# Kernel tuning notes

Measured on AMD Instinct MI355X. Metric: run time of the kernel, lower is better.

The kernel has to match this reference:

```python
import jax, jax.numpy as jnp
import numpy as np

N = 50000
E = 800000
IN = 128
HEADS = 4
C = 32  # out_features per head
HC = HEADS * C


def setup_inputs() -> dict:
    key = jax.random.key(0)
    ks = jax.random.split(key, 10)
    s_in = 1.0 / np.sqrt(IN)
    x = jax.random.normal(ks[0], (N, IN), dtype=jnp.float32)
    edge_index = jax.random.randint(ks[1], (2, E), 0, N, dtype=jnp.int64)
    Wq = jax.random.normal(ks[2], (IN, HC), dtype=jnp.float32) * s_in
    bq = jnp.zeros((HC,), dtype=jnp.float32)
    Wk = jax.random.normal(ks[3], (IN, HC), dtype=jnp.float32) * s_in
    bk = jnp.zeros((HC,), dtype=jnp.float32)
    Wv = jax.random.normal(ks[4], (IN, HC), dtype=jnp.float32) * s_in
    bv = jnp.zeros((HC,), dtype=jnp.float32)
    Wskip = jax.random.normal(ks[5], (IN, HC), dtype=jnp.float32) * s_in
    bskip = jnp.zeros((HC,), dtype=jnp.float32)
    return {"x": x, "edge_index": edge_index, "Wq": Wq, "bq": bq,
            "Wk": Wk, "bk": bk, "Wv": Wv, "bv": bv,
            "Wskip": Wskip, "bskip": bskip}


def reference(x, edge_index, Wq, bq, Wk, bk, Wv, bv, Wskip, bskip):
    src = edge_index[0]  # message source j
    dst = edge_index[1]  # message target i

    q = (x @ Wq + bq).reshape(N, HEADS, C)
    k = (x @ Wk + bk).reshape(N, HEADS, C)
    v = (x @ Wv + bv).reshape(N, HEADS, C)

    # per-edge attention logits: [E, H]
    logits = jnp.einsum('ehc,ehc->eh', q[dst], k[src]) / jnp.sqrt(
        jnp.asarray(C, dtype=x.dtype))

    # segment softmax over incoming edges of each target node
    seg_max = jax.ops.segment_max(logits, dst, num_segments=N)
    seg_max = jnp.where(jnp.isfinite(seg_max), seg_max, 0.0)
    expd = jnp.exp(logits - seg_max[dst])
    seg_sum = jax.ops.segment_sum(expd, dst, num_segments=N)
    alpha = expd / (seg_sum[dst] + 1e-16)  # [E, H]

    # scatter-add weighted values: [N, H, C]
    msgs = alpha[:, :, None] * v[src]
    out = jax.ops.segment_sum(msgs, dst, num_segments=N)
    out = out.reshape(N, HC) + (x @ Wskip + bskip)  # root/skip connection

    # LeakyReLU(negative_slope=0.2)
    return jnp.where(out >= 0, out, 0.2 * out)
```

## Files before the change

### kernel.cpp

```cpp
#include <hip/hip_runtime.h>

#define N_NODES 50000
#define E_EDGES 800000
#define IN_F 128
#define HC 128
#define NCOLS 512
#define ROWTILES 3125
#define SCAN_BLOCKS 196
#define PACK_BLOCKS 32
#define HIST_BLOCKS ((E_EDGES + 255) / 256)

typedef __attribute__((ext_vector_type(8))) short short8;
typedef __attribute__((ext_vector_type(4))) float floatx4;

__device__ __forceinline__ unsigned short f2bf(float f) {
    union { float f; unsigned u; } x; x.f = f;
    unsigned r = x.u + 0x7FFF + ((x.u >> 16) & 1);
    return (unsigned short)(r >> 16);
}
__device__ __forceinline__ float bflo(unsigned u) {
    union { unsigned u; float f; } c; c.u = u << 16; return c.f;
}
__device__ __forceinline__ float bfhi(unsigned u) {
    union { unsigned u; float f; } c; c.u = u & 0xFFFF0000u; return c.f;
}

__global__ __launch_bounds__(256) void pack_w(
    const float* __restrict__ Wq, const float* __restrict__ Wk,
    const float* __restrict__ Wv, const float* __restrict__ Ws,
    const float* __restrict__ bq, const float* __restrict__ bk,
    const float* __restrict__ bv, const float* __restrict__ bs,
    short* __restrict__ bpack, float* __restrict__ bcat,
    int* __restrict__ cnt)
{
    int t = blockIdx.x * 256 + threadIdx.x;
    int lane = t & 63, ks = (t >> 6) & 3, nt = t >> 8;
    int col = nt * 16 + (lane & 15);
    int sec = col >> 7, c = col & 127;
    const float* W = sec == 0 ? Wq : sec == 1 ? Wk : sec == 2 ? Wv : Ws;
    int kbase = ks * 32 + (lane >> 4) * 8;
    short8 b;
#pragma unroll
    for (int j = 0; j < 8; j++) b[j] = (short)f2bf(W[(size_t)(kbase + j) * HC + c]);
    *(short8*)(bpack + (size_t)t * 8) = b;
    if (t < NCOLS) {
        int s2 = t >> 7, c2 = t & 127;
        bcat[t] = (s2 == 0 ? bq : s2 == 1 ? bk : s2 == 2 ? bv : bs)[c2];
    }
    for (int i = t; i < N_NODES; i += PACK_BLOCKS * 256) cnt[i] = 0;
}

__global__ __launch_bounds__(256) void gemm_hist(
    const float* __restrict__ x, const short* __restrict__ bpack,
    const float* __restrict__ bcat,
    unsigned short* __restrict__ q, unsigned short* __restrict__ k,
    unsigned short* __restrict__ v, float* __restrict__ out,
    const int* __restrict__ dst, int* __restrict__ cnt, int* __restrict__ rank)
{
    if (blockIdx.x >= ROWTILES) {
        int e = (blockIdx.x - ROWTILES) * 256 + threadIdx.x;
        if (e < E_EDGES) rank[e] = atomicAdd(&cnt[dst[e]], 1);
        return;
    }
    __shared__ __align__(16) unsigned char lds_raw[3 * 4096 + 8192];

    const int rt = blockIdx.x;
    const int cg = threadIdx.x >> 6;
    const int lane = threadIdx.x & 63;
    const int l16 = lane & 15;
    const int m0 = rt * 16 + l16;
    const int koff = (lane >> 4) * 8;

    short8 a0[4];
#pragma unroll
    for (int ks = 0; ks < 4; ks++) {
        const float* p0 = x + (size_t)m0 * IN_F + ks * 32 + koff;
        float4 lo = *(const float4*)p0;
        float4 hi = *(const float4*)(p0 + 4);
        short8 a;
        a[0] = (short)f2bf(lo.x); a[1] = (short)f2bf(lo.y);
        a[2] = (short)f2bf(lo.z); a[3] = (short)f2bf(lo.w);
        a[4] = (short)f2bf(hi.x); a[5] = (short)f2bf(hi.y);
        a[6] = (short)f2bf(hi.z); a[7] = (short)f2bf(hi.w);
        a0[ks] = a;
    }

    unsigned short* Lb = (unsigned short*)(lds_raw + cg * 4096);
    float*          Lf = (float*)(lds_raw + 12288);
    const int rrb = (lane >> 4) * 4;

#pragma unroll
    for (int nt8 = 0; nt8 < 8; nt8++) {
        const int nt = cg * 8 + nt8;
        floatx4 acc = {0.f, 0.f, 0.f, 0.f};
#pragma unroll
        for (int ks = 0; ks < 4; ks++) {
            short8 b = *(const short8*)(bpack + ((size_t)(nt * 4 + ks) * 64 + lane) * 8);
            acc = __builtin_amdgcn_mfma_f32_16x16x32_bf16(a0[ks], b, acc, 0, 0, 0);
        }
        const int c = nt8 * 16 + l16;
        const float bias = bcat[cg * 128 + c];
        if (cg < 3) {
#pragma unroll
            for (int r = 0; r < 4; r++)
                Lb[(rrb + r) * 128 + c] = f2bf(acc[r] + bias);
        } else {
#pragma unroll
            for (int r = 0; r < 4; r++)
                Lf[(rrb + r) * 128 + c] = acc[r] + bias;
        }
    }
    __syncthreads();

    if (cg < 3) {
        unsigned short* dstb = (cg == 0) ? q : (cg == 1) ? k : v;
        unsigned short* gout = dstb + (size_t)rt * 16 * HC;
#pragma unroll
        for (int rep = 0; rep < 4; rep++) {
            int idx = rep * 64 + lane;
            *(uint4*)(gout + idx * 8) = *(const uint4*)(Lb + idx * 8);
        }
    } else {
        float* gout = out + (size_t)rt * 16 * HC;
#pragma unroll
        for (int rep = 0; rep < 8; rep++) {
            int idx = rep * 64 + lane;
            *(float4*)(gout + idx * 4) = *(const float4*)(Lf + idx * 4);
        }
    }
}

__global__ __launch_bounds__(256) void scan_apply(const int* __restrict__ cnt,
                                                  int* __restrict__ rowptr)
{
    __shared__ int wsum[4];
    const int t = threadIdx.x;
    const int lane = t & 63, w = t >> 6;
    const int limit = blockIdx.x * 256;

    int s = 0;
    for (int i = t; i < limit; i += 256) s += cnt[i];
#pragma unroll
    for (int off = 32; off >= 1; off >>= 1) s += __shfl_xor(s, off);
    if (lane == 0) wsum[w] = s;
    __syncthreads();
    const int prefix = wsum[0] + wsum[1] + wsum[2] + wsum[3];
    __syncthreads();

    int idx = limit + t;
    int val = (idx < N_NODES) ? cnt[idx] : 0;
    int incl = val;
#pragma unroll
    for (int off = 1; off < 64; off <<= 1) {
        int u = __shfl_up(incl, off);
        if (lane >= off) incl += u;
    }
    if (lane == 63) wsum[w] = incl;
    __syncthreads();
    int pre = 0;
#pragma unroll
    for (int i = 0; i < 4; i++) if (i < w) pre += wsum[i];
    int excl = prefix + pre + incl - val;
    if (idx < N_NODES) rowptr[idx] = excl;
    if (idx == N_NODES - 1) rowptr[N_NODES] = E_EDGES;
}

__global__ __launch_bounds__(256) void scatter_k(const int* __restrict__ src,
                                                 const int* __restrict__ dst,
                                                 const int* __restrict__ rowptr,
                                                 const int* __restrict__ rank,
                                                 int* __restrict__ ssrc)
{
    int e = blockIdx.x * 256 + threadIdx.x;
    if (e < E_EDGES) ssrc[rowptr[dst[e]] + rank[e]] = src[e];
}

__global__ __launch_bounds__(256) void node_attn(
    const unsigned short* __restrict__ q, const unsigned short* __restrict__ k,
    const unsigned short* __restrict__ v, const int* __restrict__ rowptr,
    const int* __restrict__ ssrc, float* __restrict__ out)
{
    const int wave = (blockIdx.x * 256 + threadIdx.x) >> 6;
    if (wave >= N_NODES) return;
    const int lane = threadIdx.x & 63;
    const int node = wave;
    const int g = lane >> 3;
    const int l8 = lane & 7;
    const int c0 = l8 * 16;

    const uint4 uq0 = *(const uint4*)(q + (size_t)node * HC + c0);
    const uint4 uq1 = *(const uint4*)(q + (size_t)node * HC + c0 + 8);

    float acc[16];
#pragma unroll
    for (int i = 0; i < 16; i++) acc[i] = 0.f;
    float ssum = 0.f;

    const int beg = __builtin_amdgcn_readfirstlane(rowptr[node]);
    const int end = __builtin_amdgcn_readfirstlane(rowptr[node + 1]);
    const float scale = 0.17677669529663687f;

    for (int e = beg; e < end; e += 8) {
        const int ee = e + g;
        const int jj = ssrc[ee < end ? ee : beg];
        const unsigned short* kp = k + (size_t)jj * HC + c0;
        const unsigned short* vp = v + (size_t)jj * HC + c0;
        const uint4 uk0 = *(const uint4*)kp;
        const uint4 uk1 = *(const uint4*)(kp + 8);
        const uint4 uv0 = *(const uint4*)vp;
        const uint4 uv1 = *(const uint4*)(vp + 8);

        float p = bflo(uq0.x) * bflo(uk0.x) + bfhi(uq0.x) * bfhi(uk0.x)
                + bflo(uq0.y) * bflo(uk0.y) + bfhi(uq0.y) * bfhi(uk0.y)
                + bflo(uq0.z) * bflo(uk0.z) + bfhi(uq0.z) * bfhi(uk0.z)
                + bflo(uq0.w) * bflo(uk0.w) + bfhi(uq0.w) * bfhi(uk0.w)
                + bflo(uq1.x) * bflo(uk1.x) + bfhi(uq1.x) * bfhi(uk1.x)
                + bflo(uq1.y) * bflo(uk1.y) + bfhi(uq1.y) * bfhi(uk1.y)
                + bflo(uq1.z) * bflo(uk1.z) + bfhi(uq1.z) * bfhi(uk1.z)
                + bflo(uq1.w) * bflo(uk1.w) + bfhi(uq1.w) * bfhi(uk1.w);
        p += __shfl_xor(p, 1);
        float wgt = __expf(p * scale);
        wgt = (ee < end) ? wgt : 0.f;
        ssum += wgt;

        acc[0]  += wgt * bflo(uv0.x); acc[1]  += wgt * bfhi(uv0.x);
        acc[2]  += wgt * bflo(uv0.y); acc[3]  += wgt * bfhi(uv0.y);
        acc[4]  += wgt * bflo(uv0.z); acc[5]  += wgt * bfhi(uv0.z);
        acc[6]  += wgt * bflo(uv0.w); acc[7]  += wgt * bfhi(uv0.w);
        acc[8]  += wgt * bflo(uv1.x); acc[9]  += wgt * bfhi(uv1.x);
        acc[10] += wgt * bflo(uv1.y); acc[11] += wgt * bfhi(uv1.y);
        acc[12] += wgt * bflo(uv1.z); acc[13] += wgt * bfhi(uv1.z);
        acc[14] += wgt * bflo(uv1.w); acc[15] += wgt * bfhi(uv1.w);
    }

    ssum += __shfl_xor(ssum, 8);
    ssum += __shfl_xor(ssum, 16);
    ssum += __shfl_xor(ssum, 32);
#pragma unroll
    for (int i = 0; i < 16; i++) {
        acc[i] += __shfl_xor(acc[i], 8);
        acc[i] += __shfl_xor(acc[i], 16);
        acc[i] += __shfl_xor(acc[i], 32);
    }

    if (g == 0) {
        const float inv = 1.0f / (ssum + 1e-16f);
        float* op = out + (size_t)node * HC + c0;
        float o[16];
#pragma unroll
        for (int i = 0; i < 16; i += 4) {
            float4 s = *(const float4*)(op + i);
            o[i]     = acc[i]     * inv + s.x;
            o[i + 1] = acc[i + 1] * inv + s.y;
            o[i + 2] = acc[i + 2] * inv + s.z;
            o[i + 3] = acc[i + 3] * inv + s.w;
        }
#pragma unroll
        for (int i = 0; i < 16; i++) o[i] = o[i] >= 0.f ? o[i] : 0.2f * o[i];
#pragma unroll
        for (int i = 0; i < 16; i += 4)
            *(float4*)(op + i) = make_float4(o[i], o[i + 1], o[i + 2], o[i + 3]);
    }
}

extern "C" void kernel_launch(void* const* d_in, const int* in_sizes, int n_in,
                              void* d_out, int out_size, void* d_ws, size_t ws_size,
                              hipStream_t stream)
{
    const float* x    = (const float*)d_in[0];
    const int*   ei   = (const int*)d_in[1];
    const float* Wq   = (const float*)d_in[2];
    const float* bq   = (const float*)d_in[3];
    const float* Wk   = (const float*)d_in[4];
    const float* bk   = (const float*)d_in[5];
    const float* Wv   = (const float*)d_in[6];
    const float* bv   = (const float*)d_in[7];
    const float* Wsk  = (const float*)d_in[8];
    const float* bsk  = (const float*)d_in[9];
    float* out = (float*)d_out;

    char* w = (char*)d_ws;
    const size_t NFB = (size_t)N_NODES * HC * sizeof(unsigned short);
    unsigned short* q = (unsigned short*)w;            w += NFB;
    unsigned short* k = (unsigned short*)w;            w += NFB;
    unsigned short* v = (unsigned short*)w;            w += NFB;
    short* bpack = (short*)w;                          w += 8192 * 8 * sizeof(short);
    float* bcat  = (float*)w;                          w += NCOLS * sizeof(float);
    int* cnt    = (int*)w;                             w += N_NODES * sizeof(int);
    int* rowptr = (int*)w;                             w += (N_NODES + 1) * sizeof(int);
    int* rank   = (int*)w;                             w += (size_t)E_EDGES * sizeof(int);
    int* ssrc   = (int*)w;

    const int* srcIdx = ei;
    const int* dstIdx = ei + E_EDGES;

    pack_w<<<PACK_BLOCKS, 256, 0, stream>>>(Wq, Wk, Wv, Wsk, bq, bk, bv, bsk,
                                            bpack, bcat, cnt);
    gemm_hist<<<ROWTILES + HIST_BLOCKS, 256, 0, stream>>>(
        x, bpack, bcat, q, k, v, out, dstIdx, cnt, rank);
    scan_apply<<<SCAN_BLOCKS, 256, 0, stream>>>(cnt, rowptr);
    scatter_k<<<(E_EDGES + 255) / 256, 256, 0, stream>>>(srcIdx, dstIdx, rowptr, rank, ssrc);
    node_attn<<<(N_NODES * 64) / 256, 256, 0, stream>>>(q, k, v, rowptr, ssrc, out);
}
```

Before: 173.8 us.

## Process four row tiles per GEMM block and move histogram into pack kernel

The projection GEMM now handles four 16-row tiles per block, loading each packed weight fragment once and reusing it across four MFMA accumulators. The skip output is written straight from registers to global memory instead of staging through LDS. The edge histogram moves into the weight-pack kernel, and the count array is cleared with a memset instead. This reduces repeated weight loads and the number of blocks, but raises register pressure and makes the fp32 output stores uncoalesced.

Result: slower. 187.4 us (+7.8%).

```diff
diff --git a/kernel.cpp b/kernel.cpp
--- a/kernel.cpp
+++ b/kernel.cpp
@@ -6,6 +6,8 @@
 #define HC 128
 #define NCOLS 512
 #define ROWTILES 3125
+#define RT_PER_BLK 4
+#define GEMM_BLOCKS 782
 #define SCAN_BLOCKS 196
 #define PACK_BLOCKS 32
 #define HIST_BLOCKS ((E_EDGES + 255) / 256)
@@ -25,107 +27,119 @@
     union { unsigned u; float f; } c; c.u = u & 0xFFFF0000u; return c.f;
 }
 
-__global__ __launch_bounds__(256) void pack_w(
+__global__ __launch_bounds__(256) void pack_hist_k(
     const float* __restrict__ Wq, const float* __restrict__ Wk,
     const float* __restrict__ Wv, const float* __restrict__ Ws,
     const float* __restrict__ bq, const float* __restrict__ bk,
     const float* __restrict__ bv, const float* __restrict__ bs,
     short* __restrict__ bpack, float* __restrict__ bcat,
-    int* __restrict__ cnt)
-{
-    int t = blockIdx.x * 256 + threadIdx.x;
-    int lane = t & 63, ks = (t >> 6) & 3, nt = t >> 8;
-    int col = nt * 16 + (lane & 15);
-    int sec = col >> 7, c = col & 127;
-    const float* W = sec == 0 ? Wq : sec == 1 ? Wk : sec == 2 ? Wv : Ws;
-    int kbase = ks * 32 + (lane >> 4) * 8;
-    short8 b;
-#pragma unroll
-    for (int j = 0; j < 8; j++) b[j] = (short)f2bf(W[(size_t)(kbase + j) * HC + c]);
-    *(short8*)(bpack + (size_t)t * 8) = b;
-    if (t < NCOLS) {
-        int s2 = t >> 7, c2 = t & 127;
-        bcat[t] = (s2 == 0 ? bq : s2 == 1 ? bk : s2 == 2 ? bv : bs)[c2];
-    }
-    for (int i = t; i < N_NODES; i += PACK_BLOCKS * 256) cnt[i] = 0;
-}
-
-__global__ __launch_bounds__(256) void gemm_hist(
+    const int* __restrict__ dst, int* __restrict__ cnt, int* __restrict__ rank)
+{
+    if (blockIdx.x < PACK_BLOCKS) {
+        int t = blockIdx.x * 256 + threadIdx.x;
+        int lane = t & 63, ks = (t >> 6) & 3, nt = t >> 8;
+        int col = nt * 16 + (lane & 15);
+        int sec = col >> 7, c = col & 127;
+        const float* W = sec == 0 ? Wq : sec == 1 ? Wk : sec == 2 ? Wv : Ws;
+        int kbase = ks * 32 + (lane >> 4) * 8;
+        short8 b;
+#pragma unroll
+        for (int j = 0; j < 8; j++) b[j] = (short)f2bf(W[(size_t)(kbase + j) * HC + c]);
+        *(short8*)(bpack + (size_t)t * 8) = b;
+        if (t < NCOLS) {
+            int s2 = t >> 7, c2 = t & 127;
+            bcat[t] = (s2 == 0 ? bq : s2 == 1 ? bk : s2 == 2 ? bv : bs)[c2];
+        }
+    } else {
+        int e = (blockIdx.x - PACK_BLOCKS) * 256 + threadIdx.x;
+        if (e < E_EDGES) rank[e] = atomicAdd(&cnt[dst[e]], 1);
+    }
+}
+
+__global__ __launch_bounds__(256, 3) void gemm_mfma(
     const float* __restrict__ x, const short* __restrict__ bpack,
     const float* __restrict__ bcat,
     unsigned short* __restrict__ q, unsigned short* __restrict__ k,
-    unsigned short* __restrict__ v, float* __restrict__ out,
-    const int* __restrict__ dst, int* __restrict__ cnt, int* __restrict__ rank)
-{
-    if (blockIdx.x >= ROWTILES) {
-        int e = (blockIdx.x - ROWTILES) * 256 + threadIdx.x;
-        if (e < E_EDGES) rank[e] = atomicAdd(&cnt[dst[e]], 1);
-        return;
-    }
-    __shared__ __align__(16) unsigned char lds_raw[3 * 4096 + 8192];
-
-    const int rt = blockIdx.x;
+    unsigned short* __restrict__ v, float* __restrict__ out)
+{
+    __shared__ unsigned short Lb[3][RT_PER_BLK][16 * 128];
+
     const int cg = threadIdx.x >> 6;
     const int lane = threadIdx.x & 63;
     const int l16 = lane & 15;
-    const int m0 = rt * 16 + l16;
     const int koff = (lane >> 4) * 8;
-
-    short8 a0[4];
-#pragma unroll
-    for (int ks = 0; ks < 4; ks++) {
-        const float* p0 = x + (size_t)m0 * IN_F + ks * 32 + koff;
-        float4 lo = *(const float4*)p0;
-        float4 hi = *(const float4*)(p0 + 4);
-        short8 a;
-        a[0] = (short)f2bf(lo.x); a[1] = (short)f2bf(lo.y);
-        a[2] = (short)f2bf(lo.z); a[3] = (short)f2bf(lo.w);
-        a[4] = (short)f2bf(hi.x); a[5] = (short)f2bf(hi.y);
-        a[6] = (short)f2bf(hi.z); a[7] = (short)f2bf(hi.w);
-        a0[ks] = a;
-    }
-
-    unsigned short* Lb = (unsigned short*)(lds_raw + cg * 4096);
-    float*          Lf = (float*)(lds_raw + 12288);
     const int rrb = (lane >> 4) * 4;
+    const int rt0 = blockIdx.x * RT_PER_BLK;
+
+    short8 a[RT_PER_BLK][4];
+#pragma unroll
+    for (int rtl = 0; rtl < RT_PER_BLK; rtl++) {
+        int row = (rt0 + rtl) * 16 + l16;
+        if (row >= N_NODES) row = N_NODES - 1;
+#pragma unroll
+        for (int ks = 0; ks < 4; ks++) {
+            const float* p0 = x + (size_t)row * IN_F + ks * 32 + koff;
+            float4 lo = *(const float4*)p0;
+            float4 hi = *(const float4*)(p0 + 4);
+            short8 aa;
+            aa[0] = (short)f2bf(lo.x); aa[1] = (short)f2bf(lo.y);
+            aa[2] = (short)f2bf(lo.z); aa[3] = (short)f2bf(lo.w);
+            aa[4] = (short)f2bf(hi.x); aa[5] = (short)f2bf(hi.y);
+            aa[6] = (short)f2bf(hi.z); aa[7] = (short)f2bf(hi.w);
+            a[rtl][ks] = aa;
+        }
+    }
 
 #pragma unroll
     for (int nt8 = 0; nt8 < 8; nt8++) {
         const int nt = cg * 8 + nt8;
-        floatx4 acc = {0.f, 0.f, 0.f, 0.f};
-#pragma unroll
-        for (int ks = 0; ks < 4; ks++) {
-            short8 b = *(const short8*)(bpack + ((size_t)(nt * 4 + ks) * 64 + lane) * 8);
-            acc = __builtin_amdgcn_mfma_f32_16x16x32_bf16(a0[ks], b, acc, 0, 0, 0);
-        }
+        short8 b[4];
+#pragma unroll
+        for (int ks = 0; ks < 4; ks++)
+            b[ks] = *(const short8*)(bpack + ((size_t)(nt * 4 + ks) * 64 + lane) * 8);
+
+        floatx4 acc[RT_PER_BLK];
+#pragma unroll
+        for (int rtl = 0; rtl < RT_PER_BLK; rtl++) acc[rtl] = {0.f, 0.f, 0.f, 0.f};
+#pragma unroll
+        for (int ks = 0; ks < 4; ks++)
+#pragma unroll
+            for (int rtl = 0; rtl < RT_PER_BLK; rtl++)
+                acc[rtl] = __builtin_amdgcn_mfma_f32_16x16x32_bf16(a[rtl][ks], b[ks], acc[rtl], 0, 0, 0);
+
         const int c = nt8 * 16 + l16;
         const float bias = bcat[cg * 128 + c];
         if (cg < 3) {
 #pragma unroll
-            for (int r = 0; r < 4; r++)
-                Lb[(rrb + r) * 128 + c] = f2bf(acc[r] + bias);
+            for (int rtl = 0; rtl < RT_PER_BLK; rtl++)
+#pragma unroll
+                for (int r = 0; r < 4; r++)
+                    Lb[cg][rtl][(rrb + r) * 128 + c] = f2bf(acc[rtl][r] + bias);
         } else {
 #pragma unroll
-            for (int r = 0; r < 4; r++)
-                Lf[(rrb + r) * 128 + c] = acc[r] + bias;
-        }
-    }
-    __syncthreads();
+            for (int rtl = 0; rtl < RT_PER_BLK; rtl++) {
+                if (rt0 + rtl < ROWTILES) {
+                    const int rbase = (rt0 + rtl) * 16 + rrb;
+#pragma unroll
+                    for (int r = 0; r < 4; r++)
+                        out[(size_t)(rbase + r) * HC + c] = acc[rtl][r] + bias;
+                }
+            }
+        }
+    }
 
     if (cg < 3) {
         unsigned short* dstb = (cg == 0) ? q : (cg == 1) ? k : v;
-        unsigned short* gout = dstb + (size_t)rt * 16 * HC;
-#pragma unroll
-        for (int rep = 0; rep < 4; rep++) {
-            int idx = rep * 64 + lane;
-            *(uint4*)(gout + idx * 8) = *(const uint4*)(Lb + idx * 8);
-        }
-    } else {
-        float* gout = out + (size_t)rt * 16 * HC;
-#pragma unroll
-        for (int rep = 0; rep < 8; rep++) {
-            int idx = rep * 64 + lane;
-            *(float4*)(gout + idx * 4) = *(const float4*)(Lf + idx * 4);
+#pragma unroll
+        for (int rtl = 0; rtl < RT_PER_BLK; rtl++) {
+            if (rt0 + rtl < ROWTILES) {
+                unsigned short* gout = dstb + (size_t)(rt0 + rtl) * 16 * HC;
+#pragma unroll
+                for (int rep = 0; rep < 4; rep++) {
+                    int idx = rep * 64 + lane;
+                    *(uint4*)(gout + idx * 8) = *(const uint4*)(&Lb[cg][rtl][idx * 8]);
+                }
+            }
         }
     }
 }
@@ -294,10 +308,10 @@
     const int* srcIdx = ei;
     const int* dstIdx = ei + E_EDGES;
 
-    pack_w<<<PACK_BLOCKS, 256, 0, stream>>>(Wq, Wk, Wv, Wsk, bq, bk, bv, bsk,
-                                            bpack, bcat, cnt);
-    gemm_hist<<<ROWTILES + HIST_BLOCKS, 256, 0, stream>>>(
-        x, bpack, bcat, q, k, v, out, dstIdx, cnt, rank);
+    hipMemsetAsync(cnt, 0, N_NODES * sizeof(int), stream);
+    pack_hist_k<<<PACK_BLOCKS + HIST_BLOCKS, 256, 0, stream>>>(
+        Wq, Wk, Wv, Wsk, bq, bk, bv, bsk, bpack, bcat, dstIdx, cnt, rank);
+    gemm_mfma<<<GEMM_BLOCKS, 256, 0, stream>>>(x, bpack, bcat, q, k, v, out);
     scan_apply<<<SCAN_BLOCKS, 256, 0, stream>>>(cnt, rowptr);
     scatter_k<<<(E_EDGES + 255) / 256, 256, 0, stream>>>(srcIdx, dstIdx, rowptr, rank, ssrc);
     node_attn<<<(N_NODES * 64) / 256, 256, 0, stream>>>(q, k, v, rowptr, ssrc, out);
```
